# Kernel optimization log

Hardware: AMD Instinct MI355X
Metric: run time of the kernel (lower is better)

Reference implementation:

```python
import jax, jax.numpy as jnp
import numpy as np

SHIFT = 1  # module picks random +-1 at init; fixed deterministically to +1


def setup_inputs() -> dict:
    key = jax.random.key(0)
    k1, k2, k3 = jax.random.split(key, 3)
    x = jax.random.normal(k1, (128, 128, 56, 56), dtype=jnp.float32)
    w0 = jax.random.normal(k2, (2, 3, 3, 32), dtype=jnp.float32)
    w1 = jax.random.normal(k3, (64, 4), dtype=jnp.float32)
    return {"x": x, "w0": w0, "w1": w1}


def _unfold3(t, axis):
    # F.unfold with kernel (3,1), padding (1,0) along `axis` (length 56):
    # zero-pad by 1 on each side, then stack the 3 shifted windows as a new
    # axis placed just BEFORE `axis` (matching torch's C*kh channel ordering
    # after the reshapes in the original module).
    pad = [(0, 0)] * t.ndim
    pad[axis] = (1, 1)
    p = jnp.pad(t, pad)
    slices = []
    for a in range(3):
        idx = [slice(None)] * t.ndim
        idx[axis] = slice(a, a + 56)
        slices.append(p[tuple(idx)])
    return jnp.stack(slices, axis=axis)


def reference(x, w0, w1):
    # x: (128,128,56,56) -> (k=128, j=64, m=2, n=56, l=56)
    t3 = x.reshape(128, 64, 2, 56, 56)
    # channel mix: contract j=64 against w1 (64,4) -> (b, m=2, n=56, l=56, i=4)
    t4 = jnp.einsum('kjmnl,ji->kmnli', t3, w1)
    # first unfold over l (axis 3): (b, 2, 56, kA=3, l=56, i=4)
    u1 = _unfold3(t4, axis=3)
    # second unfold over l again (now axis 4), padding applied to u1 (which
    # already contains zeros from the first padding) -> (b,2,56,kA,kB,l,i)
    u2 = _unfold3(u1, axis=4)
    # torch permute (0,1,2,5,4,3,6): (b, 2, 56, l, kB, kA, i)
    t5 = jnp.transpose(u2, (0, 1, 2, 5, 4, 3, 6))
    # conv-like contraction with w0 (l=2, i=3, k=3, j=32) -> (b,56,56,4,32)
    t6 = jnp.einsum('mlonikp,likj->monpj', t5, w0)
    # (b,56,56,32,4) -> (b,56,56,128), roll along H, -> NCHW
    t7 = jnp.transpose(t6, (0, 1, 2, 4, 3)).reshape(128, 56, 56, 128)
    t7 = jnp.roll(t7, SHIFT, axis=1)
    return jnp.transpose(t7, (0, 3, 1, 2))
```

## Files before the change

kernel.cpp:

```cpp
#include <hip/hip_runtime.h>

namespace {
constexpr int CH = 128, HH = 56, WW = 56;

__global__ __launch_bounds__(256, 4) void fused_conv_kernel(
    const float* __restrict__ x,
    const float* __restrict__ w0,
    const float* __restrict__ w1,
    float* __restrict__ out)
{
    __shared__ float xs[CH * WW];
    __shared__ float t4s[4][2][57];
    __shared__ float w0s[2 * 3 * 3 * 32];
    __shared__ float w1s[64 * 4];

    const int tid = threadIdx.x;
    const int b   = blockIdx.x / HH;
    const int h   = blockIdx.x % HH;

    for (int t = tid; t < 576; t += 256) w0s[t] = w0[t];
    if (tid < 256) w1s[tid] = w1[tid];

    const size_t chan_stride = (size_t)HH * WW;
    const float* xrow = x + ((size_t)b * CH * HH + h) * WW;

    #pragma unroll
    for (int it = 0; it < 7; ++it) {
        int t  = it * 256 + tid;
        int ch = t / 14;
        int q  = t - ch * 14;
        float4 v = *reinterpret_cast<const float4*>(xrow + (size_t)ch * chan_stride + q * 4);
        *reinterpret_cast<float4*>(&xs[ch * WW + q * 4]) = v;
    }
    __syncthreads();

    for (int idx = tid; idx < 448; idx += 256) {
        int m = idx & 1;
        int l = (idx >> 1) % 56;
        int i = idx / 112;
        float acc = 0.f;
        #pragma unroll
        for (int j = 0; j < 64; ++j)
            acc = fmaf(xs[(2 * j + m) * WW + l], w1s[j * 4 + i], acc);
        t4s[i][m][l] = acc;
    }
    __syncthreads();

    const int h_out = (h + 1) % HH;
    float* orow = out + ((size_t)b * CH * HH + h_out) * WW;
    #pragma unroll
    for (int it = 0; it < 7; ++it) {
        int t  = it * 256 + tid;
        int c  = t / 14;
        int q  = t - c * 14;
        int l0 = q * 4;
        int j  = c >> 2;
        int i  = c & 3;

        float vals[2][8];
        #pragma unroll
        for (int m = 0; m < 2; ++m)
            #pragma unroll
            for (int d = 0; d < 8; ++d) {
                int lsrc = l0 - 2 + d;
                vals[m][d] = (lsrc >= 0 && lsrc < WW) ? t4s[i][m][lsrc] : 0.f;
            }

        float acc0 = 0.f, acc1 = 0.f, acc2 = 0.f, acc3 = 0.f;
        #pragma unroll
        for (int m = 0; m < 2; ++m)
            #pragma unroll
            for (int kB = 0; kB < 3; ++kB)
                #pragma unroll
                for (int kA = 0; kA < 3; ++kA) {
                    float wv = w0s[((m * 3 + kB) * 3 + kA) * 32 + j];
                    int dd = kA + kB;
                    acc0 = fmaf(vals[m][dd],     wv, acc0);
                    acc1 = fmaf(vals[m][dd + 1], wv, acc1);
                    acc2 = fmaf(vals[m][dd + 2], wv, acc2);
                    acc3 = fmaf(vals[m][dd + 3], wv, acc3);
                }

        if (l0 == 0) {
            #pragma unroll
            for (int m = 0; m < 2; ++m)
                acc0 -= t4s[i][m][0] * w0s[((m * 3 + 0) * 3 + 2) * 32 + j];
        }
        if (l0 == 52) {
            #pragma unroll
            for (int m = 0; m < 2; ++m)
                acc3 -= t4s[i][m][55] * w0s[((m * 3 + 2) * 3 + 0) * 32 + j];
        }

        float4 res = make_float4(acc0, acc1, acc2, acc3);
        *reinterpret_cast<float4*>(orow + (size_t)c * chan_stride + l0) = res;
    }
}
}

extern "C" void kernel_launch(void* const* d_in, const int* in_sizes, int n_in,
                              void* d_out, int out_size, void* d_ws, size_t ws_size,
                              hipStream_t stream) {
    const float* x  = (const float*)d_in[0];
    const float* w0 = (const float*)d_in[1];
    const float* w1 = (const float*)d_in[2];
    float* out = (float*)d_out;
    fused_conv_kernel<<<dim3(128 * 56), dim3(256), 0, stream>>>(x, w0, w1, out);
}
```

Before: 117.0 us.

## Compute channel mix directly from global memory, two rows per block

Drops the 28 KB shared-memory staging of the input row and has each thread compute the 64-channel mix for one output position straight from global memory, keeping all four mixed outputs in registers. Each block now handles two H rows. The mixed buffer is zero-padded with a padded row length so the conv stage can use aligned float4 shared loads without bounds checks. The smaller LDS footprint allows a higher occupancy hint. The risk is that the strided global loads in the mix stage, done by only 224 threads, expose more latency than the old coalesced float4 staging did.

```diff
diff --git a/kernel.cpp b/kernel.cpp
--- a/kernel.cpp
+++ b/kernel.cpp
@@ -2,98 +2,109 @@
 
 namespace {
 constexpr int CH = 128, HH = 56, WW = 56;
+constexpr int R  = 2;
+constexpr int LP = 60;
 
-__global__ __launch_bounds__(256, 4) void fused_conv_kernel(
+__global__ __launch_bounds__(256, 6) void fused_conv_kernel(
     const float* __restrict__ x,
     const float* __restrict__ w0,
     const float* __restrict__ w1,
     float* __restrict__ out)
 {
-    __shared__ float xs[CH * WW];
-    __shared__ float t4s[4][2][57];
+    __shared__ float t4s[R][2][4][LP];
     __shared__ float w0s[2 * 3 * 3 * 32];
-    __shared__ float w1s[64 * 4];
 
     const int tid = threadIdx.x;
-    const int b   = blockIdx.x / HH;
-    const int h   = blockIdx.x % HH;
+    const int b   = blockIdx.x / (HH / R);
+    const int hg  = blockIdx.x - b * (HH / R);
+    const int h0  = hg * R;
 
     for (int t = tid; t < 576; t += 256) w0s[t] = w0[t];
-    if (tid < 256) w1s[tid] = w1[tid];
 
-    const size_t chan_stride = (size_t)HH * WW;
-    const float* xrow = x + ((size_t)b * CH * HH + h) * WW;
+    if (tid < R * 32) {
+        int e = tid;
+        const int r = e >> 5; e &= 31;
+        const int m = e >> 4; e &= 15;
+        const int i = e >> 2;
+        const int p = e & 3;
+        t4s[r][m][i][(p < 2) ? p : (56 + p)] = 0.f;
+    }
 
-    #pragma unroll
-    for (int it = 0; it < 7; ++it) {
-        int t  = it * 256 + tid;
-        int ch = t / 14;
-        int q  = t - ch * 14;
-        float4 v = *reinterpret_cast<const float4*>(xrow + (size_t)ch * chan_stride + q * 4);
-        *reinterpret_cast<float4*>(&xs[ch * WW + q * 4]) = v;
+    if (tid < R * 112) {
+        int e = tid;
+        const int r = e / 112; e -= r * 112;
+        const int m = e / 56;
+        const int l = e - m * 56;
+        const float*  xp  = x + (((size_t)b * CH + m) * HH + (h0 + r)) * WW + l;
+        const float4* w1v = (const float4*)w1;
+        float a0 = 0.f, a1 = 0.f, a2 = 0.f, a3 = 0.f;
+        #pragma unroll 8
+        for (int j = 0; j < 64; ++j) {
+            const float  xv = xp[(size_t)j * (2 * HH * WW)];
+            const float4 wv = w1v[j];
+            a0 = fmaf(xv, wv.x, a0);
+            a1 = fmaf(xv, wv.y, a1);
+            a2 = fmaf(xv, wv.z, a2);
+            a3 = fmaf(xv, wv.w, a3);
+        }
+        t4s[r][m][0][2 + l] = a0;
+        t4s[r][m][1][2 + l] = a1;
+        t4s[r][m][2][2 + l] = a2;
+        t4s[r][m][3][2 + l] = a3;
     }
     __syncthreads();
 
-    for (int idx = tid; idx < 448; idx += 256) {
-        int m = idx & 1;
-        int l = (idx >> 1) % 56;
-        int i = idx / 112;
-        float acc = 0.f;
-        #pragma unroll
-        for (int j = 0; j < 64; ++j)
-            acc = fmaf(xs[(2 * j + m) * WW + l], w1s[j * 4 + i], acc);
-        t4s[i][m][l] = acc;
-    }
-    __syncthreads();
+    #pragma unroll 2
+    for (int it = 0; it < R * 7; ++it) {
+        const int t  = it * 256 + tid;
+        const int r  = t / 1792;
+        const int tt = t - r * 1792;
+        const int c  = tt / 14;
+        const int q  = tt - c * 14;
+        const int l0 = q * 4;
+        const int j  = c >> 2;
+        const int i  = c & 3;
 
-    const int h_out = (h + 1) % HH;
-    float* orow = out + ((size_t)b * CH * HH + h_out) * WW;
-    #pragma unroll
-    for (int it = 0; it < 7; ++it) {
-        int t  = it * 256 + tid;
-        int c  = t / 14;
-        int q  = t - c * 14;
-        int l0 = q * 4;
-        int j  = c >> 2;
-        int i  = c & 3;
-
-        float vals[2][8];
-        #pragma unroll
-        for (int m = 0; m < 2; ++m)
-            #pragma unroll
-            for (int d = 0; d < 8; ++d) {
-                int lsrc = l0 - 2 + d;
-                vals[m][d] = (lsrc >= 0 && lsrc < WW) ? t4s[i][m][lsrc] : 0.f;
-            }
+        const float* tp0 = &t4s[r][0][i][l0];
+        const float* tp1 = &t4s[r][1][i][l0];
+        const float4 p0a = *(const float4*)(tp0);
+        const float4 p0b = *(const float4*)(tp0 + 4);
+        const float4 p1a = *(const float4*)(tp1);
+        const float4 p1b = *(const float4*)(tp1 + 4);
+        const float v0[8] = {p0a.x, p0a.y, p0a.z, p0a.w, p0b.x, p0b.y, p0b.z, p0b.w};
+        const float v1[8] = {p1a.x, p1a.y, p1a.z, p1a.w, p1b.x, p1b.y, p1b.z, p1b.w};
 
         float acc0 = 0.f, acc1 = 0.f, acc2 = 0.f, acc3 = 0.f;
         #pragma unroll
-        for (int m = 0; m < 2; ++m)
+        for (int m = 0; m < 2; ++m) {
             #pragma unroll
-            for (int kB = 0; kB < 3; ++kB)
+            for (int kB = 0; kB < 3; ++kB) {
                 #pragma unroll
                 for (int kA = 0; kA < 3; ++kA) {
-                    float wv = w0s[((m * 3 + kB) * 3 + kA) * 32 + j];
-                    int dd = kA + kB;
-                    acc0 = fmaf(vals[m][dd],     wv, acc0);
-                    acc1 = fmaf(vals[m][dd + 1], wv, acc1);
-                    acc2 = fmaf(vals[m][dd + 2], wv, acc2);
-                    acc3 = fmaf(vals[m][dd + 3], wv, acc3);
+                    const float wv = w0s[((m * 3 + kB) * 3 + kA) * 32 + j];
+                    const int dd = kA + kB;
+                    acc0 = fmaf(m ? v1[dd]     : v0[dd],     wv, acc0);
+                    acc1 = fmaf(m ? v1[dd + 1] : v0[dd + 1], wv, acc1);
+                    acc2 = fmaf(m ? v1[dd + 2] : v0[dd + 2], wv, acc2);
+                    acc3 = fmaf(m ? v1[dd + 3] : v0[dd + 3], wv, acc3);
                 }
+            }
+        }
 
         if (l0 == 0) {
             #pragma unroll
             for (int m = 0; m < 2; ++m)
-                acc0 -= t4s[i][m][0] * w0s[((m * 3 + 0) * 3 + 2) * 32 + j];
+                acc0 -= t4s[r][m][i][2] * w0s[((m * 3 + 0) * 3 + 2) * 32 + j];
         }
         if (l0 == 52) {
             #pragma unroll
             for (int m = 0; m < 2; ++m)
-                acc3 -= t4s[i][m][55] * w0s[((m * 3 + 2) * 3 + 0) * 32 + j];
+                acc3 -= t4s[r][m][i][57] * w0s[((m * 3 + 2) * 3 + 0) * 32 + j];
         }
 
-        float4 res = make_float4(acc0, acc1, acc2, acc3);
-        *reinterpret_cast<float4*>(orow + (size_t)c * chan_stride + l0) = res;
+        const int h_out = (h0 + r + 1) % HH;
+        float* orow = out + (((size_t)b * CH + c) * HH + h_out) * WW + l0;
+        *(float4*)orow = make_float4(acc0, acc1, acc2, acc3);
     }
 }
 }
@@ -105,5 +116,5 @@
     const float* w0 = (const float*)d_in[1];
     const float* w1 = (const float*)d_in[2];
     float* out = (float*)d_out;
-    fused_conv_kernel<<<dim3(128 * 56), dim3(256), 0, stream>>>(x, w0, w1, out);
+    fused_conv_kernel<<<dim3(128 * (HH / R)), dim3(256), 0, stream>>>(x, w0, w1, out);
 }
```

Result: slower. 121.9 us (+4.3%).

## Split fused kernel into channel-mix and conv kernels with collapsed 5-tap filter

Applied to the files above, without the earlier changes.

Splits the single fused kernel into two. The first computes the 64-to-4 channel mix with register-tiled float4 loads straight from global memory and writes a small intermediate to workspace. The second loads that intermediate for 14 rows into padded shared memory and applies the two stacked 3-tap unfolds, algebraically folded into one 5-tap filter with edge corrections. Each conv block covers 8 output channel groups. This removes the per-row shared staging of the full input and the redundant 9-tap FMAs, at the cost of an extra launch and an intermediate round-trip through global memory.

```diff
diff --git a/kernel.cpp b/kernel.cpp
--- a/kernel.cpp
+++ b/kernel.cpp
@@ -1,99 +1,167 @@
 #include <hip/hip_runtime.h>
 
 namespace {
-constexpr int CH = 128, HH = 56, WW = 56;
+constexpr int HH = 56, WW = 56;
+constexpr int CPLANE = HH * WW;
+constexpr int LSTRIDE = 516;
 
-__global__ __launch_bounds__(256, 4) void fused_conv_kernel(
+__global__ __launch_bounds__(128, 2) void chanmix_kernel(
     const float* __restrict__ x,
+    const float* __restrict__ w1,
+    float* __restrict__ t4g)
+{
+    __shared__ float4 w1s[64];
+    const int tid = threadIdx.x;
+    if (tid < 64) w1s[tid] = ((const float4*)w1)[tid];
+    __syncthreads();
+
+    const int b  = blockIdx.x >> 3;
+    const int hg = blockIdx.x & 7;
+    const int h0 = hg * 7;
+
+    if (tid >= 98) return;
+    const int rh = tid / 14;
+    const int wq = tid - rh * 14;
+    const int h  = h0 + rh;
+
+    const float* xp = x + ((size_t)b * 128 * HH + h) * WW + wq * 4;
+
+    float acc[2][4][4];
+    #pragma unroll
+    for (int m = 0; m < 2; ++m)
+        #pragma unroll
+        for (int i = 0; i < 4; ++i)
+            #pragma unroll
+            for (int q = 0; q < 4; ++q) acc[m][i][q] = 0.f;
+
+    #pragma unroll 2
+    for (int ch0 = 0; ch0 < 128; ch0 += 8) {
+        float4 xv[8];
+        #pragma unroll
+        for (int k = 0; k < 8; ++k)
+            xv[k] = *(const float4*)(xp + (size_t)(ch0 + k) * CPLANE);
+        #pragma unroll
+        for (int k = 0; k < 8; ++k) {
+            const int m = k & 1;
+            const float4 wv = w1s[(ch0 + k) >> 1];
+            const float xk[4] = {xv[k].x, xv[k].y, xv[k].z, xv[k].w};
+            const float wk[4] = {wv.x, wv.y, wv.z, wv.w};
+            #pragma unroll
+            for (int i = 0; i < 4; ++i)
+                #pragma unroll
+                for (int q = 0; q < 4; ++q)
+                    acc[m][i][q] = fmaf(xk[q], wk[i], acc[m][i][q]);
+        }
+    }
+
+    float* tp = t4g + (size_t)(b * HH + h) * 448 + wq * 4;
+    #pragma unroll
+    for (int m = 0; m < 2; ++m)
+        #pragma unroll
+        for (int i = 0; i < 4; ++i)
+            *(float4*)(tp + (m * 4 + i) * WW) =
+                make_float4(acc[m][i][0], acc[m][i][1], acc[m][i][2], acc[m][i][3]);
+}
+
+__global__ __launch_bounds__(256, 2) void conv_kernel(
+    const float* __restrict__ t4g,
     const float* __restrict__ w0,
-    const float* __restrict__ w1,
     float* __restrict__ out)
 {
-    __shared__ float xs[CH * WW];
-    __shared__ float t4s[4][2][57];
-    __shared__ float w0s[2 * 3 * 3 * 32];
-    __shared__ float w1s[64 * 4];
+    __shared__ float ls[14 * LSTRIDE];
+    __shared__ float w0s[576];
 
     const int tid = threadIdx.x;
-    const int b   = blockIdx.x / HH;
-    const int h   = blockIdx.x % HH;
+    const int cg  = blockIdx.x & 3;
+    const int hg  = (blockIdx.x >> 2) & 3;
+    const int b   = blockIdx.x >> 4;
+    const int h0  = hg * 14;
 
     for (int t = tid; t < 576; t += 256) w0s[t] = w0[t];
-    if (tid < 256) w1s[tid] = w1[tid];
 
-    const size_t chan_stride = (size_t)HH * WW;
-    const float* xrow = x + ((size_t)b * CH * HH + h) * WW;
+    if (tid < 224) {
+        const int row  = tid >> 1;
+        const int half = tid & 1;
+        const int hh = row >> 3, mi = row & 7;
+        *(float2*)&ls[hh * LSTRIDE + mi * 64 + (half ? 58 : 0)] = make_float2(0.f, 0.f);
+    }
 
+    const float4* src = (const float4*)(t4g + (size_t)(b * HH + h0) * 448);
     #pragma unroll
-    for (int it = 0; it < 7; ++it) {
-        int t  = it * 256 + tid;
-        int ch = t / 14;
-        int q  = t - ch * 14;
-        float4 v = *reinterpret_cast<const float4*>(xrow + (size_t)ch * chan_stride + q * 4);
-        *reinterpret_cast<float4*>(&xs[ch * WW + q * 4]) = v;
+    for (int k = 0; k < 7; ++k) {
+        const int idx = k * 256 + tid;
+        if (idx < 1568) {
+            const float4 v = src[idx];
+            const int row = idx / 14, wq = idx - row * 14;
+            const int hh = row >> 3, mi = row & 7;
+            float* d = &ls[hh * LSTRIDE + mi * 64 + 2 + 4 * wq];
+            *(float2*)d       = make_float2(v.x, v.y);
+            *(float2*)(d + 2) = make_float2(v.z, v.w);
+        }
     }
     __syncthreads();
 
-    for (int idx = tid; idx < 448; idx += 256) {
-        int m = idx & 1;
-        int l = (idx >> 1) % 56;
-        int i = idx / 112;
-        float acc = 0.f;
+    if (tid >= 196) return;
+    const int rh = tid / 14;
+    const int wq = tid - rh * 14;
+    const int l0 = 4 * wq;
+
+    float v[2][4][8];
+    #pragma unroll
+    for (int m = 0; m < 2; ++m)
         #pragma unroll
-        for (int j = 0; j < 64; ++j)
-            acc = fmaf(xs[(2 * j + m) * WW + l], w1s[j * 4 + i], acc);
-        t4s[i][m][l] = acc;
-    }
-    __syncthreads();
+        for (int i = 0; i < 4; ++i) {
+            const float* p = &ls[rh * LSTRIDE + (m * 4 + i) * 64 + l0];
+            const float4 p0 = *(const float4*)p;
+            const float4 p1 = *(const float4*)(p + 4);
+            v[m][i][0] = p0.x; v[m][i][1] = p0.y; v[m][i][2] = p0.z; v[m][i][3] = p0.w;
+            v[m][i][4] = p1.x; v[m][i][5] = p1.y; v[m][i][6] = p1.z; v[m][i][7] = p1.w;
+        }
 
-    const int h_out = (h + 1) % HH;
-    float* orow = out + ((size_t)b * CH * HH + h_out) * WW;
-    #pragma unroll
-    for (int it = 0; it < 7; ++it) {
-        int t  = it * 256 + tid;
-        int c  = t / 14;
-        int q  = t - c * 14;
-        int l0 = q * 4;
-        int j  = c >> 2;
-        int i  = c & 3;
+    const int h_out = (h0 + rh + 1) % HH;
+    float* obase = out + ((size_t)b * 128 * HH + h_out) * WW + l0;
 
-        float vals[2][8];
+    #pragma unroll 2
+    for (int jj = 0; jj < 8; ++jj) {
+        const int j = cg * 8 + jj;
+        float W[2][5], fix0[2], fix3[2];
         #pragma unroll
-        for (int m = 0; m < 2; ++m)
-            #pragma unroll
-            for (int d = 0; d < 8; ++d) {
-                int lsrc = l0 - 2 + d;
-                vals[m][d] = (lsrc >= 0 && lsrc < WW) ? t4s[i][m][lsrc] : 0.f;
-            }
-
-        float acc0 = 0.f, acc1 = 0.f, acc2 = 0.f, acc3 = 0.f;
+        for (int m = 0; m < 2; ++m) {
+            const float w00 = w0s[((m * 3 + 0) * 3 + 0) * 32 + j];
+            const float w01 = w0s[((m * 3 + 0) * 3 + 1) * 32 + j];
+            const float w02 = w0s[((m * 3 + 0) * 3 + 2) * 32 + j];
+            const float w10 = w0s[((m * 3 + 1) * 3 + 0) * 32 + j];
+            const float w11 = w0s[((m * 3 + 1) * 3 + 1) * 32 + j];
+            const float w12 = w0s[((m * 3 + 1) * 3 + 2) * 32 + j];
+            const float w20 = w0s[((m * 3 + 2) * 3 + 0) * 32 + j];
+            const float w21 = w0s[((m * 3 + 2) * 3 + 1) * 32 + j];
+            const float w22 = w0s[((m * 3 + 2) * 3 + 2) * 32 + j];
+            W[m][0] = w00;
+            W[m][1] = w01 + w10;
+            W[m][2] = w02 + w11 + w20;
+            W[m][3] = w12 + w21;
+            W[m][4] = w22;
+            fix0[m] = w02;
+            fix3[m] = w20;
+        }
         #pragma unroll
-        for (int m = 0; m < 2; ++m)
-            #pragma unroll
-            for (int kB = 0; kB < 3; ++kB)
-                #pragma unroll
-                for (int kA = 0; kA < 3; ++kA) {
-                    float wv = w0s[((m * 3 + kB) * 3 + kA) * 32 + j];
-                    int dd = kA + kB;
-                    acc0 = fmaf(vals[m][dd],     wv, acc0);
-                    acc1 = fmaf(vals[m][dd + 1], wv, acc1);
-                    acc2 = fmaf(vals[m][dd + 2], wv, acc2);
-                    acc3 = fmaf(vals[m][dd + 3], wv, acc3);
-                }
-
-        if (l0 == 0) {
+        for (int i = 0; i < 4; ++i) {
+            float o0 = 0.f, o1 = 0.f, o2 = 0.f, o3 = 0.f;
             #pragma unroll
             for (int m = 0; m < 2; ++m)
-                acc0 -= t4s[i][m][0] * w0s[((m * 3 + 0) * 3 + 2) * 32 + j];
+                #pragma unroll
+                for (int d = 0; d < 5; ++d) {
+                    const float wd = W[m][d];
+                    o0 = fmaf(v[m][i][d],     wd, o0);
+                    o1 = fmaf(v[m][i][d + 1], wd, o1);
+                    o2 = fmaf(v[m][i][d + 2], wd, o2);
+                    o3 = fmaf(v[m][i][d + 3], wd, o3);
+                }
+            if (wq == 0)  o0 -= v[0][i][2] * fix0[0] + v[1][i][2] * fix0[1];
+            if (wq == 13) o3 -= v[0][i][5] * fix3[0] + v[1][i][5] * fix3[1];
+            const int c = j * 4 + i;
+            *(float4*)(obase + (size_t)c * CPLANE) = make_float4(o0, o1, o2, o3);
         }
-        if (l0 == 52) {
-            #pragma unroll
-            for (int m = 0; m < 2; ++m)
-                acc3 -= t4s[i][m][55] * w0s[((m * 3 + 2) * 3 + 0) * 32 + j];
-        }
-
-        float4 res = make_float4(acc0, acc1, acc2, acc3);
-        *reinterpret_cast<float4*>(orow + (size_t)c * chan_stride + l0) = res;
     }
 }
 }
@@ -105,5 +173,8 @@
     const float* w0 = (const float*)d_in[1];
     const float* w1 = (const float*)d_in[2];
     float* out = (float*)d_out;
-    fused_conv_kernel<<<dim3(128 * 56), dim3(256), 0, stream>>>(x, w0, w1, out);
+    float* t4g = (float*)d_ws;
+
+    chanmix_kernel<<<dim3(128 * 8), dim3(128), 0, stream>>>(x, w1, t4g);
+    conv_kernel<<<dim3(128 * 16), dim3(256), 0, stream>>>(t4g, w0, out);
 }
```

Measured after the change: 150.5 us. 28.6% more time.
